# Kernel tuning notes

Measured on AMD Instinct MI355X. Metric: run time of the kernel, lower is better.

Reference implementation:

```python
import jax, jax.numpy as jnp
import numpy as np

D = 512          # embedding_dim (cfg.hidden_size)
K = 1024         # codebook_size
DECAY = 0.99
EPS = 1e-05
COMMITMENT_COST = 0.25


def setup_inputs() -> dict:
    key = jax.random.key(0)
    k1, k2, k3 = jax.random.split(key, 3)
    return {
        "inputs": jax.random.normal(k1, (32, 1024, D), dtype=jnp.float32),
        "embedding_weight": jax.random.normal(k2, (K, D), dtype=jnp.float32),
        "ema_cluster_size": jnp.zeros((K,), dtype=jnp.float32),
        "ema_w": jax.random.normal(k3, (K, D), dtype=jnp.float32),
    }


def reference(inputs, embedding_weight, ema_cluster_size, ema_w):
    input_shape = inputs.shape
    flat = inputs.reshape(-1, D)  # [N, D]

    # Squared L2 distances to every codebook entry: [N, K]
    distances = (
        jnp.sum(flat ** 2, axis=1, keepdims=True)
        + jnp.sum(embedding_weight ** 2, axis=1)
        - 2.0 * flat @ embedding_weight.T
    )
    idx = jnp.argmin(distances, axis=1)                      # [N]
    encodings = jax.nn.one_hot(idx, K, dtype=flat.dtype)     # [N, K]

    # ---- EMA codebook update (training path) ----
    counts = jnp.sum(encodings, axis=0)                      # == bincount(idx)
    new_cs = ema_cluster_size * DECAY + (1.0 - DECAY) * counts
    n = jnp.sum(new_cs)
    new_cs = (new_cs + EPS) / (n + K * EPS) * n              # Laplace smoothing
    # dw = encodings.T @ flat, done as a fused gather-reduce instead of dense matmul
    dw = jax.ops.segment_sum(flat, idx, num_segments=K)      # [K, D]
    new_ema_w = ema_w * DECAY + (1.0 - DECAY) * dw
    new_embedding = new_ema_w / new_cs[:, None]              # updated codebook

    # quantized = encodings @ new_embedding, expressed as a gather
    quantized = new_embedding[idx].reshape(input_shape)

    e_latent_loss = jnp.mean((jax.lax.stop_gradient(quantized) - inputs) ** 2)
    loss = COMMITMENT_COST * e_latent_loss

    # straight-through estimator
    quantized = inputs + jax.lax.stop_gradient(quantized - inputs)

    avg_probs = jnp.mean(encodings, axis=0)
    perplexity = jnp.exp(-jnp.sum(avg_probs * jnp.log(avg_probs + 1e-10)))
    return (loss, quantized, perplexity, encodings)
```

## Files before the change

### kernel.cpp

```cpp
#include <hip/hip_runtime.h>

#define NROWS 32768
#define DIM   512
#define KC    1024

typedef __attribute__((ext_vector_type(8)))  short short8v;
typedef __attribute__((ext_vector_type(16))) float f32x16;

__global__ __launch_bounds__(256) void k_enorm(const float* __restrict__ E,
                                               float* __restrict__ en2) {
    int w = threadIdx.x >> 6, lane = threadIdx.x & 63;
    int c = blockIdx.x * 4 + w;
    const float* row = E + (size_t)c * DIM;
    float4 a = *reinterpret_cast<const float4*>(&row[lane * 8]);
    float4 b = *reinterpret_cast<const float4*>(&row[lane * 8 + 4]);
    float s = a.x*a.x + a.y*a.y + a.z*a.z + a.w*a.w
            + b.x*b.x + b.y*b.y + b.z*b.z + b.w*b.w;
    #pragma unroll
    for (int off = 32; off; off >>= 1) s += __shfl_xor(s, off);
    if (!lane) en2[c] = s;
}

__device__ __forceinline__ void split_bf16(float v, short& hi, short& lo) {
    unsigned u = __float_as_uint(v);
    unsigned r = u + 0x7FFFu + ((u >> 16) & 1u);
    hi = (short)(r >> 16);
    float hif = __uint_as_float(r & 0xFFFF0000u);
    float rem = v - hif;
    unsigned u2 = __float_as_uint(rem);
    unsigned r2 = u2 + 0x7FFFu + ((u2 >> 16) & 1u);
    lo = (short)(r2 >> 16);
}

__device__ __forceinline__ unsigned long long pack_key(float d, int c) {
    unsigned u = __float_as_uint(d);
    u = (u & 0x80000000u) ? ~u : (u | 0x80000000u);
    return ((unsigned long long)u << 32) | (unsigned)c;
}

__global__ __launch_bounds__(256) void k_split(const float* __restrict__ x,
                                               const float* __restrict__ E,
                                               short* __restrict__ xfrag,
                                               short* __restrict__ efrag) {
    __shared__ short hbuf[32][520];
    __shared__ short lbuf[32][520];
    int b = blockIdx.x, t = threadIdx.x;
    const float* src;
    short* dst;
    if (b < NROWS / 32) {
        src = x + (size_t)b * 32 * DIM;
        dst = xfrag + (size_t)b * 32768;
    } else {
        src = E + (size_t)(b - NROWS / 32) * 32 * DIM;
        dst = efrag + (size_t)(b - NROWS / 32) * 32768;
    }
    #pragma unroll
    for (int f = 0; f < 16; ++f) {
        int u = t + f * 256;
        int row = u >> 7, c4 = (u & 127) * 4;
        float4 v = *reinterpret_cast<const float4*>(&src[row * DIM + c4]);
        short4 h4, l4;
        split_bf16(v.x, h4.x, l4.x); split_bf16(v.y, h4.y, l4.y);
        split_bf16(v.z, h4.z, l4.z); split_bf16(v.w, h4.w, l4.w);
        *reinterpret_cast<short4*>(&hbuf[row][c4]) = h4;
        *reinterpret_cast<short4*>(&lbuf[row][c4]) = l4;
    }
    __syncthreads();
    #pragma unroll
    for (int f = 0; f < 16; ++f) {
        int u = t + f * 256;
        int lane = u & 63, h = (u >> 6) & 1, kb = u >> 7;
        int row = lane & 31, k0 = kb * 16 + (lane >> 5) * 8;
        const short* s = h ? &lbuf[row][k0] : &hbuf[row][k0];
        short8v val = *reinterpret_cast<const short8v*>(s);
        *reinterpret_cast<short8v*>(&dst[(size_t)u * 8]) = val;
    }
}

__global__ __launch_bounds__(256, 3) void k_argmin(const short* __restrict__ xfrag,
                                                   const short* __restrict__ efrag,
                                                   const float* __restrict__ en2,
                                                   unsigned long long* __restrict__ packed) {
    const int tid = threadIdx.x;
    const int w = tid >> 6, l = tid & 63;
    const int wr = w >> 1, wc = w & 1;
    const int l31 = l & 31, lh = l >> 5;

    int bid = blockIdx.x;
    int xcd = bid & 7, j = bid >> 3;
    int row0 = (xcd * 32 + (j >> 3)) * 128;
    int c0   = (j & 7) * 128;

    const short* ab[2];
    const short* bb[2];
    #pragma unroll
    for (int tm = 0; tm < 2; ++tm)
        ab[tm] = xfrag + (size_t)(row0 / 32 + wr * 2 + tm) * 32768 + l * 8;
    #pragma unroll
    for (int tn = 0; tn < 2; ++tn)
        bb[tn] = efrag + (size_t)(c0 / 32 + wc * 2 + tn) * 32768 + l * 8;

    f32x16 acc[2][2];
    #pragma unroll
    for (int a = 0; a < 2; ++a)
        #pragma unroll
        for (int b = 0; b < 2; ++b)
            #pragma unroll
            for (int r = 0; r < 16; ++r) acc[a][b][r] = 0.f;

    #pragma unroll 2
    for (int kb = 0; kb < 32; ++kb) {
        short8v axh[2], axl[2], beh[2], bel[2];
        #pragma unroll
        for (int tm = 0; tm < 2; ++tm) {
            axh[tm] = *reinterpret_cast<const short8v*>(ab[tm] + kb * 1024);
            axl[tm] = *reinterpret_cast<const short8v*>(ab[tm] + kb * 1024 + 512);
        }
        #pragma unroll
        for (int tn = 0; tn < 2; ++tn) {
            beh[tn] = *reinterpret_cast<const short8v*>(bb[tn] + kb * 1024);
            bel[tn] = *reinterpret_cast<const short8v*>(bb[tn] + kb * 1024 + 512);
        }
        #pragma unroll
        for (int tm = 0; tm < 2; ++tm)
            #pragma unroll
            for (int tn = 0; tn < 2; ++tn) {
                acc[tm][tn] = __builtin_amdgcn_mfma_f32_32x32x16_bf16(
                    axh[tm], beh[tn], acc[tm][tn], 0, 0, 0);
                acc[tm][tn] = __builtin_amdgcn_mfma_f32_32x32x16_bf16(
                    axh[tm], bel[tn], acc[tm][tn], 0, 0, 0);
                acc[tm][tn] = __builtin_amdgcn_mfma_f32_32x32x16_bf16(
                    axl[tm], beh[tn], acc[tm][tn], 0, 0, 0);
            }
    }

    float e2[2];
    #pragma unroll
    for (int tn = 0; tn < 2; ++tn) e2[tn] = en2[c0 + wc * 64 + tn * 32 + l31];
    const int cA = c0 + wc * 64 + l31;
    #pragma unroll
    for (int tm = 0; tm < 2; ++tm) {
        #pragma unroll
        for (int r = 0; r < 16; ++r) {
            float d0 = fmaf(-2.f, acc[tm][0][r], e2[0]);
            float d1 = fmaf(-2.f, acc[tm][1][r], e2[1]);
            unsigned long long k0 = pack_key(d0, cA);
            unsigned long long k1 = pack_key(d1, cA + 32);
            unsigned long long key = k0 < k1 ? k0 : k1;
            #pragma unroll
            for (int off = 1; off < 32; off <<= 1) {
                unsigned long long o = __shfl_xor(key, off);
                if (o < key) key = o;
            }
            if (l31 == 0) {
                int grow = row0 + wr * 64 + tm * 32 + (r & 3) + 8 * (r >> 2) + 4 * lh;
                atomicMin(&packed[grow], key);
            }
        }
    }
}

__global__ __launch_bounds__(256) void k_hist(const unsigned long long* __restrict__ packed,
                                              int* __restrict__ idx,
                                              int* __restrict__ counts) {
    __shared__ int h[KC];
    for (int i = threadIdx.x; i < KC; i += 256) h[i] = 0;
    __syncthreads();
    int g = blockIdx.x * 256 + threadIdx.x;
    int c = (int)(unsigned)(packed[g] & 0xFFFFFFFFull);
    idx[g] = c;
    atomicAdd(&h[c], 1);
    __syncthreads();
    for (int i = threadIdx.x; i < KC; i += 256)
        if (h[i]) atomicAdd(&counts[i], h[i]);
}

__global__ __launch_bounds__(1024) void k_meta(const int* __restrict__ counts,
                                               const float* __restrict__ ema_cs,
                                               float* __restrict__ smoothed,
                                               int* __restrict__ offsets,
                                               int* __restrict__ cursor,
                                               float* __restrict__ perp_out) {
    __shared__ float red[KC];
    __shared__ int sc[KC];
    int t = threadIdx.x;
    int cnt = counts[t];
    float cs = ema_cs[t] * 0.99f + 0.01f * (float)cnt;
    red[t] = cs; __syncthreads();
    for (int s = 512; s; s >>= 1) { if (t < s) red[t] += red[t + s]; __syncthreads(); }
    float n = red[0];
    __syncthreads();
    float sm = (cs + 1e-5f) / (n + 1024.f * 1e-5f) * n;
    smoothed[t] = sm;
    float p = (float)cnt / 32768.f;
    red[t] = p * logf(p + 1e-10f);
    __syncthreads();
    for (int s = 512; s; s >>= 1) { if (t < s) red[t] += red[t + s]; __syncthreads(); }
    if (!t) perp_out[0] = expf(-red[0]);
    sc[t] = cnt; __syncthreads();
    for (int s = 1; s < KC; s <<= 1) {
        int v = (t >= s) ? sc[t - s] : 0;
        __syncthreads();
        sc[t] += v;
        __syncthreads();
    }
    int off = sc[t] - cnt;
    offsets[t] = off;
    cursor[t] = off;
}

__global__ __launch_bounds__(256) void k_scatter(const int* __restrict__ idx,
                                                 int* __restrict__ cursor,
                                                 int* __restrict__ bucket) {
    int g = blockIdx.x * 256 + threadIdx.x;
    int c = idx[g];
    int pos = atomicAdd(&cursor[c], 1);
    bucket[pos] = g;
}

__global__ __launch_bounds__(256) void k_enc(const int* __restrict__ idx,
                                             float* __restrict__ enc) {
    int t = threadIdx.x;
    int row = blockIdx.x * 8 + (t >> 5);
    int l32 = t & 31;
    int one = idx[row];
    float4* dst = reinterpret_cast<float4*>(enc + (size_t)row * KC);
    #pragma unroll
    for (int s = 0; s < 8; ++s) {
        int c4 = l32 + s * 32;
        int base = c4 * 4;
        float4 v;
        v.x = (one == base)     ? 1.f : 0.f;
        v.y = (one == base + 1) ? 1.f : 0.f;
        v.z = (one == base + 2) ? 1.f : 0.f;
        v.w = (one == base + 3) ? 1.f : 0.f;
        dst[c4] = v;
    }
}

__global__ __launch_bounds__(256) void k_dw(const float* __restrict__ x,
                                            const float* __restrict__ ema_w,
                                            const int* __restrict__ offsets,
                                            const int* __restrict__ counts,
                                            const int* __restrict__ bucket,
                                            const float* __restrict__ smoothed,
                                            float* __restrict__ newE) {
    __shared__ int rows[256];
    int k = blockIdx.x, t = threadIdx.x;
    int beg = offsets[k], m = counts[k];
    float a0 = 0.f, a1 = 0.f;
    for (int base = 0; base < m; base += 256) {
        int n = min(256, m - base);
        __syncthreads();
        if (t < n) rows[t] = bucket[beg + base + t];
        __syncthreads();
        int i = 0;
        for (; i + 4 <= n; i += 4) {
            int r0 = rows[i], r1 = rows[i + 1], r2 = rows[i + 2], r3 = rows[i + 3];
            float v00 = x[(size_t)r0 * DIM + t];
            float v01 = x[(size_t)r0 * DIM + t + 256];
            float v10 = x[(size_t)r1 * DIM + t];
            float v11 = x[(size_t)r1 * DIM + t + 256];
            float v20 = x[(size_t)r2 * DIM + t];
            float v21 = x[(size_t)r2 * DIM + t + 256];
            float v30 = x[(size_t)r3 * DIM + t];
            float v31 = x[(size_t)r3 * DIM + t + 256];
            a0 += v00 + v10 + v20 + v30;
            a1 += v01 + v11 + v21 + v31;
        }
        for (; i < n; ++i) {
            int r = rows[i];
            a0 += x[(size_t)r * DIM + t];
            a1 += x[(size_t)r * DIM + t + 256];
        }
    }
    float sm = smoothed[k];
    newE[(size_t)k * DIM + t]       = (ema_w[(size_t)k * DIM + t]       * 0.99f + 0.01f * a0) / sm;
    newE[(size_t)k * DIM + t + 256] = (ema_w[(size_t)k * DIM + t + 256] * 0.99f + 0.01f * a1) / sm;
}

__global__ __launch_bounds__(256) void k_quant(const float* __restrict__ x,
                                               const int* __restrict__ idx,
                                               const float* __restrict__ newE,
                                               float* __restrict__ outq,
                                               float* __restrict__ partials) {
    int t0 = blockIdx.x * 256 + threadIdx.x;
    float lp = 0.f;
    #pragma unroll 4
    for (int s = 0; s < 16; ++s) {
        int e = t0 + s * 1048576;
        int row = e >> 9;
        int c = idx[row];
        float in = x[e];
        float q = newE[(size_t)c * DIM + (e & 511)];
        float d = q - in;
        outq[e] = in + d;
        lp += d * d;
    }
    #pragma unroll
    for (int off = 32; off; off >>= 1) lp += __shfl_xor(lp, off);
    __shared__ float wr[4];
    int lane = threadIdx.x & 63, w = threadIdx.x >> 6;
    if (!lane) wr[w] = lp;
    __syncthreads();
    if (threadIdx.x == 0) partials[blockIdx.x] = wr[0] + wr[1] + wr[2] + wr[3];
}

__global__ __launch_bounds__(256) void k_lossfin(const float* __restrict__ partials,
                                                 float* __restrict__ out0) {
    __shared__ double red[256];
    double s = 0.0;
    for (int i = threadIdx.x; i < 4096; i += 256) s += (double)partials[i];
    red[threadIdx.x] = s; __syncthreads();
    for (int st = 128; st; st >>= 1) {
        if (threadIdx.x < st) red[threadIdx.x] += red[threadIdx.x + st];
        __syncthreads();
    }
    if (!threadIdx.x) out0[0] = (float)(0.25 * red[0] / 16777216.0);
}

extern "C" void kernel_launch(void* const* d_in, const int* in_sizes, int n_in,
                              void* d_out, int out_size, void* d_ws, size_t ws_size,
                              hipStream_t stream) {
    const float* x   = (const float*)d_in[0];
    const float* E   = (const float*)d_in[1];
    const float* ecs = (const float*)d_in[2];
    const float* emw = (const float*)d_in[3];
    float* out = (float*)d_out;

    char* ws = (char*)d_ws;
    int*   idx      = (int*)(ws + 0);
    int*   bucket   = (int*)(ws + 131072);
    float* en2      = (float*)(ws + 262144);
    int*   counts   = (int*)(ws + 266240);
    int*   offsets  = (int*)(ws + 270336);
    int*   cursor   = (int*)(ws + 274432);
    float* smoothed = (float*)(ws + 278528);
    float* newE     = (float*)(ws + 282624);
    float* partials = (float*)(ws + 282624 + 2097152);
    unsigned long long* packed = (unsigned long long*)newE;

    float* out_loss = out;
    float* out_q    = out + 1;
    float* out_perp = out + 16777217;
    float* out_enc  = out + 16777218;

    short* xfrag = (short*)out_enc;
    short* efrag = xfrag + (size_t)NROWS * DIM * 2;

    hipMemsetAsync(counts, 0, KC * sizeof(int), stream);
    hipMemsetAsync(packed, 0xFF, NROWS * sizeof(unsigned long long), stream);

    k_enorm  <<<KC / 4, 256, 0, stream>>>(E, en2);
    k_split  <<<NROWS / 32 + KC / 32, 256, 0, stream>>>(x, E, xfrag, efrag);
    k_argmin <<<(NROWS / 128) * 8, 256, 0, stream>>>(xfrag, efrag, en2, packed);
    k_hist   <<<NROWS / 256, 256, 0, stream>>>(packed, idx, counts);
    k_meta   <<<1, 1024, 0, stream>>>(counts, ecs, smoothed, offsets, cursor, out_perp);
    k_scatter<<<NROWS / 256, 256, 0, stream>>>(idx, cursor, bucket);
    k_enc    <<<NROWS / 8, 256, 0, stream>>>(idx, out_enc);
    k_dw     <<<KC, 256, 0, stream>>>(x, emw, offsets, counts, bucket, smoothed, newE);
    k_quant  <<<4096, 256, 0, stream>>>(x, idx, newE, out_q, partials);
    k_lossfin<<<1, 256, 0, stream>>>(partials, out_loss);
}
```

Before: 340.7 us.

## Stage argmin GEMM tiles through double-buffered LDS and fuse one-hot into quantize

The distance GEMM kernel now stages each k-slice of the X and codebook bf16 hi/lo fragments into a double-buffered shared-memory buffer. Each block covers 128 rows by 256 codes instead of 128 by 128, so each wave reuses A fragments across four B tiles and the grid is half the size. The intent is to cut redundant global/L2 fragment loads and overlap the next slice's load with the MFMA work. The cost is 48 KB of LDS, more accumulator registers, a lower occupancy hint and a barrier per iteration. Separately, the one-hot encoding write is folded into a row-oriented, float4-vectorized quantize/loss kernel, which removes one launch and reuses the idx loads.

```diff
diff --git a/kernel.cpp b/kernel.cpp
--- a/kernel.cpp
+++ b/kernel.cpp
@@ -77,10 +77,11 @@
     }
 }
 
-__global__ __launch_bounds__(256, 3) void k_argmin(const short* __restrict__ xfrag,
+__global__ __launch_bounds__(256, 2) void k_argmin(const short* __restrict__ xfrag,
                                                    const short* __restrict__ efrag,
                                                    const float* __restrict__ en2,
                                                    unsigned long long* __restrict__ packed) {
+    __shared__ short sbuf[2][24 * 512];
     const int tid = threadIdx.x;
     const int w = tid >> 6, l = tid & 63;
     const int wr = w >> 1, wc = w & 1;
@@ -88,72 +89,105 @@
 
     int bid = blockIdx.x;
     int xcd = bid & 7, j = bid >> 3;
-    int row0 = (xcd * 32 + (j >> 3)) * 128;
-    int c0   = (j & 7) * 128;
-
-    const short* ab[2];
-    const short* bb[2];
-    #pragma unroll
-    for (int tm = 0; tm < 2; ++tm)
-        ab[tm] = xfrag + (size_t)(row0 / 32 + wr * 2 + tm) * 32768 + l * 8;
-    #pragma unroll
-    for (int tn = 0; tn < 2; ++tn)
-        bb[tn] = efrag + (size_t)(c0 / 32 + wc * 2 + tn) * 32768 + l * 8;
-
-    f32x16 acc[2][2];
+    int row0 = (xcd * 32 + (j >> 2)) * 128;
+    int c0   = (j & 3) * 256;
+
+    const short* srcbase[6];
+    #pragma unroll
+    for (int s = 0; s < 6; ++s) {
+        int q = s * 4 + (tid >> 6);
+        int g = q >> 1, h = q & 1;
+        const short* base = (g < 4)
+            ? xfrag + (size_t)(row0 / 32 + g) * 32768
+            : efrag + (size_t)(c0 / 32 + (g - 4)) * 32768;
+        srcbase[s] = base + h * 512 + (tid & 63) * 8;
+    }
+    const int stq = tid >> 6;
+    const int stl = (tid & 63) * 8;
+
+    f32x16 acc[2][4];
     #pragma unroll
     for (int a = 0; a < 2; ++a)
         #pragma unroll
-        for (int b = 0; b < 2; ++b)
+        for (int b = 0; b < 4; ++b)
             #pragma unroll
             for (int r = 0; r < 16; ++r) acc[a][b][r] = 0.f;
 
-    #pragma unroll 2
+    {
+        short8v st[6];
+        #pragma unroll
+        for (int s = 0; s < 6; ++s)
+            st[s] = *reinterpret_cast<const short8v*>(srcbase[s]);
+        #pragma unroll
+        for (int s = 0; s < 6; ++s)
+            *reinterpret_cast<short8v*>(&sbuf[0][(s * 4 + stq) * 512 + stl]) = st[s];
+    }
+    __syncthreads();
+
     for (int kb = 0; kb < 32; ++kb) {
-        short8v axh[2], axl[2], beh[2], bel[2];
-        #pragma unroll
-        for (int tm = 0; tm < 2; ++tm) {
-            axh[tm] = *reinterpret_cast<const short8v*>(ab[tm] + kb * 1024);
-            axl[tm] = *reinterpret_cast<const short8v*>(ab[tm] + kb * 1024 + 512);
-        }
-        #pragma unroll
-        for (int tn = 0; tn < 2; ++tn) {
-            beh[tn] = *reinterpret_cast<const short8v*>(bb[tn] + kb * 1024);
-            bel[tn] = *reinterpret_cast<const short8v*>(bb[tn] + kb * 1024 + 512);
-        }
-        #pragma unroll
-        for (int tm = 0; tm < 2; ++tm)
-            #pragma unroll
-            for (int tn = 0; tn < 2; ++tn) {
-                acc[tm][tn] = __builtin_amdgcn_mfma_f32_32x32x16_bf16(
-                    axh[tm], beh[tn], acc[tm][tn], 0, 0, 0);
-                acc[tm][tn] = __builtin_amdgcn_mfma_f32_32x32x16_bf16(
-                    axh[tm], bel[tn], acc[tm][tn], 0, 0, 0);
-                acc[tm][tn] = __builtin_amdgcn_mfma_f32_32x32x16_bf16(
-                    axl[tm], beh[tn], acc[tm][tn], 0, 0, 0);
+        const int cur = kb & 1;
+        short8v st[6];
+        if (kb < 31) {
+            #pragma unroll
+            for (int s = 0; s < 6; ++s)
+                st[s] = *reinterpret_cast<const short8v*>(
+                    srcbase[s] + (size_t)(kb + 1) * 1024);
+        }
+        short8v ah[2], al[2], bh[4], bl[4];
+        const short* sb = sbuf[cur];
+        #pragma unroll
+        for (int m = 0; m < 2; ++m) {
+            int g = wr * 2 + m;
+            ah[m] = *reinterpret_cast<const short8v*>(&sb[(g * 2 + 0) * 512 + l * 8]);
+            al[m] = *reinterpret_cast<const short8v*>(&sb[(g * 2 + 1) * 512 + l * 8]);
+        }
+        #pragma unroll
+        for (int n = 0; n < 4; ++n) {
+            int g = 4 + wc * 4 + n;
+            bh[n] = *reinterpret_cast<const short8v*>(&sb[(g * 2 + 0) * 512 + l * 8]);
+            bl[n] = *reinterpret_cast<const short8v*>(&sb[(g * 2 + 1) * 512 + l * 8]);
+        }
+        #pragma unroll
+        for (int m = 0; m < 2; ++m)
+            #pragma unroll
+            for (int n = 0; n < 4; ++n) {
+                acc[m][n] = __builtin_amdgcn_mfma_f32_32x32x16_bf16(
+                    ah[m], bh[n], acc[m][n], 0, 0, 0);
+                acc[m][n] = __builtin_amdgcn_mfma_f32_32x32x16_bf16(
+                    ah[m], bl[n], acc[m][n], 0, 0, 0);
+                acc[m][n] = __builtin_amdgcn_mfma_f32_32x32x16_bf16(
+                    al[m], bh[n], acc[m][n], 0, 0, 0);
             }
-    }
-
-    float e2[2];
-    #pragma unroll
-    for (int tn = 0; tn < 2; ++tn) e2[tn] = en2[c0 + wc * 64 + tn * 32 + l31];
-    const int cA = c0 + wc * 64 + l31;
-    #pragma unroll
-    for (int tm = 0; tm < 2; ++tm) {
+        if (kb < 31) {
+            #pragma unroll
+            for (int s = 0; s < 6; ++s)
+                *reinterpret_cast<short8v*>(
+                    &sbuf[cur ^ 1][(s * 4 + stq) * 512 + stl]) = st[s];
+        }
+        __syncthreads();
+    }
+
+    float e2[4];
+    #pragma unroll
+    for (int n = 0; n < 4; ++n) e2[n] = en2[c0 + wc * 128 + n * 32 + l31];
+    #pragma unroll
+    for (int m = 0; m < 2; ++m) {
         #pragma unroll
         for (int r = 0; r < 16; ++r) {
-            float d0 = fmaf(-2.f, acc[tm][0][r], e2[0]);
-            float d1 = fmaf(-2.f, acc[tm][1][r], e2[1]);
-            unsigned long long k0 = pack_key(d0, cA);
-            unsigned long long k1 = pack_key(d1, cA + 32);
-            unsigned long long key = k0 < k1 ? k0 : k1;
+            unsigned long long key = 0xFFFFFFFFFFFFFFFFull;
+            #pragma unroll
+            for (int n = 0; n < 4; ++n) {
+                float d = fmaf(-2.f, acc[m][n][r], e2[n]);
+                unsigned long long k = pack_key(d, c0 + wc * 128 + n * 32 + l31);
+                if (k < key) key = k;
+            }
             #pragma unroll
             for (int off = 1; off < 32; off <<= 1) {
                 unsigned long long o = __shfl_xor(key, off);
                 if (o < key) key = o;
             }
             if (l31 == 0) {
-                int grow = row0 + wr * 64 + tm * 32 + (r & 3) + 8 * (r >> 2) + 4 * lh;
+                int grow = row0 + wr * 64 + m * 32 + (r & 3) + 8 * (r >> 2) + 4 * lh;
                 atomicMin(&packed[grow], key);
             }
         }
@@ -218,26 +252,6 @@
     bucket[pos] = g;
 }
 
-__global__ __launch_bounds__(256) void k_enc(const int* __restrict__ idx,
-                                             float* __restrict__ enc) {
-    int t = threadIdx.x;
-    int row = blockIdx.x * 8 + (t >> 5);
-    int l32 = t & 31;
-    int one = idx[row];
-    float4* dst = reinterpret_cast<float4*>(enc + (size_t)row * KC);
-    #pragma unroll
-    for (int s = 0; s < 8; ++s) {
-        int c4 = l32 + s * 32;
-        int base = c4 * 4;
-        float4 v;
-        v.x = (one == base)     ? 1.f : 0.f;
-        v.y = (one == base + 1) ? 1.f : 0.f;
-        v.z = (one == base + 2) ? 1.f : 0.f;
-        v.w = (one == base + 3) ? 1.f : 0.f;
-        dst[c4] = v;
-    }
-}
-
 __global__ __launch_bounds__(256) void k_dw(const float* __restrict__ x,
                                             const float* __restrict__ ema_w,
                                             const int* __restrict__ offsets,
@@ -279,31 +293,55 @@
     newE[(size_t)k * DIM + t + 256] = (ema_w[(size_t)k * DIM + t + 256] * 0.99f + 0.01f * a1) / sm;
 }
 
-__global__ __launch_bounds__(256) void k_quant(const float* __restrict__ x,
-                                               const int* __restrict__ idx,
-                                               const float* __restrict__ newE,
-                                               float* __restrict__ outq,
-                                               float* __restrict__ partials) {
-    int t0 = blockIdx.x * 256 + threadIdx.x;
+__global__ __launch_bounds__(256) void k_qe(const float* __restrict__ x,
+                                            const int* __restrict__ idx,
+                                            const float* __restrict__ newE,
+                                            float* __restrict__ outq,
+                                            float* __restrict__ enc,
+                                            float* __restrict__ partials) {
+    int b = blockIdx.x, t = threadIdx.x;
+    int row8 = b * 8;
     float lp = 0.f;
-    #pragma unroll 4
-    for (int s = 0; s < 16; ++s) {
-        int e = t0 + s * 1048576;
-        int row = e >> 9;
-        int c = idx[row];
-        float in = x[e];
-        float q = newE[(size_t)c * DIM + (e & 511)];
-        float d = q - in;
-        outq[e] = in + d;
-        lp += d * d;
+    #pragma unroll
+    for (int it = 0; it < 4; ++it) {
+        int slot = t + it * 256;
+        int r = slot >> 7;
+        int c4 = (slot & 127) * 4;
+        int row = row8 + r;
+        int code = idx[row];
+        float4 in = *reinterpret_cast<const float4*>(&x[(size_t)row * DIM + c4]);
+        float4 q  = *reinterpret_cast<const float4*>(&newE[(size_t)code * DIM + c4]);
+        float4 d;
+        d.x = q.x - in.x; d.y = q.y - in.y; d.z = q.z - in.z; d.w = q.w - in.w;
+        float4 o;
+        o.x = in.x + d.x; o.y = in.y + d.y; o.z = in.z + d.z; o.w = in.w + d.w;
+        *reinterpret_cast<float4*>(&outq[(size_t)row * DIM + c4]) = o;
+        lp += d.x*d.x + d.y*d.y + d.z*d.z + d.w*d.w;
+    }
+    {
+        int er = row8 + (t >> 5);
+        int l32 = t & 31;
+        int one = idx[er];
+        float4* dst = reinterpret_cast<float4*>(enc + (size_t)er * KC);
+        #pragma unroll
+        for (int s = 0; s < 8; ++s) {
+            int c4 = l32 + s * 32;
+            int base = c4 * 4;
+            float4 v;
+            v.x = (one == base)     ? 1.f : 0.f;
+            v.y = (one == base + 1) ? 1.f : 0.f;
+            v.z = (one == base + 2) ? 1.f : 0.f;
+            v.w = (one == base + 3) ? 1.f : 0.f;
+            dst[c4] = v;
+        }
     }
     #pragma unroll
     for (int off = 32; off; off >>= 1) lp += __shfl_xor(lp, off);
     __shared__ float wr[4];
-    int lane = threadIdx.x & 63, w = threadIdx.x >> 6;
+    int lane = t & 63, w = t >> 6;
     if (!lane) wr[w] = lp;
     __syncthreads();
-    if (threadIdx.x == 0) partials[blockIdx.x] = wr[0] + wr[1] + wr[2] + wr[3];
+    if (t == 0) partials[b] = wr[0] + wr[1] + wr[2] + wr[3];
 }
 
 __global__ __launch_bounds__(256) void k_lossfin(const float* __restrict__ partials,
@@ -353,12 +391,11 @@
 
     k_enorm  <<<KC / 4, 256, 0, stream>>>(E, en2);
     k_split  <<<NROWS / 32 + KC / 32, 256, 0, stream>>>(x, E, xfrag, efrag);
-    k_argmin <<<(NROWS / 128) * 8, 256, 0, stream>>>(xfrag, efrag, en2, packed);
+    k_argmin <<<(NROWS / 128) * 4, 256, 0, stream>>>(xfrag, efrag, en2, packed);
     k_hist   <<<NROWS / 256, 256, 0, stream>>>(packed, idx, counts);
     k_meta   <<<1, 1024, 0, stream>>>(counts, ecs, smoothed, offsets, cursor, out_perp);
     k_scatter<<<NROWS / 256, 256, 0, stream>>>(idx, cursor, bucket);
-    k_enc    <<<NROWS / 8, 256, 0, stream>>>(idx, out_enc);
     k_dw     <<<KC, 256, 0, stream>>>(x, emw, offsets, counts, bucket, smoothed, newE);
-    k_quant  <<<4096, 256, 0, stream>>>(x, idx, newE, out_q, partials);
+    k_qe     <<<NROWS / 8, 256, 0, stream>>>(x, idx, newE, out_q, out_enc, partials);
     k_lossfin<<<1, 256, 0, stream>>>(partials, out_loss);
 }
```

Result: faster. 314.7 us (-7.6%).
